# Kernel optimization log

Measured on AMD Instinct MI355X. Metric: run time of the kernel, lower is better.

## Reference

```python
import jax, jax.numpy as jnp
import numpy as np
import math

B, S, H = 2, 4096, 768
NH, HD = 12, 64  # num heads, head dim


def setup_inputs() -> dict:
    key = jax.random.key(0)
    ks = jax.random.split(key, 4)
    scale = 1.0 / math.sqrt(H)
    return {
        "hidden_states": jax.random.normal(ks[0], (B, S, H), jnp.float32),
        "attention_mask": jnp.zeros((B, 1, 1, S), jnp.float32),
        "Wq": jax.random.normal(ks[1], (H, H), jnp.float32) * scale,
        "bq": jnp.zeros((H,), jnp.float32),
        "Wk": jax.random.normal(ks[2], (H, H), jnp.float32) * scale,
        "bk": jnp.zeros((H,), jnp.float32),
        "Wv": jax.random.normal(ks[3], (H, H), jnp.float32) * scale,
        "bv": jnp.zeros((H,), jnp.float32),
    }


def reference(hidden_states, attention_mask, Wq, bq, Wk, bk, Wv, bv):
    # Linear projections (torch nn.Linear: x @ W.T + b)
    q = hidden_states @ Wq.T + bq  # [B,S,H]
    k = hidden_states @ Wk.T + bk
    v = hidden_states @ Wv.T + bv
    # split heads -> [B, NH, S, HD]
    def split(x):
        return x.reshape(B, S, NH, HD).transpose(0, 2, 1, 3)
    qh, kh, vh = split(q), split(k), split(v)
    scores = jnp.einsum('bhqd,bhkd->bhqk', qh, kh) / math.sqrt(HD)
    scores = scores + attention_mask  # additive mask, broadcast
    probs = jax.nn.softmax(scores, axis=-1)
    # dropout prob = 0.0 (inference) -> identity
    ctx = jnp.einsum('bhqk,bhkd->bhqd', probs, vh)
    ctx = ctx.transpose(0, 2, 1, 3).reshape(B, S, H)
    return ctx
```

## Files before the change

kernel.cpp:

```cpp
#include <hip/hip_runtime.h>
#include <hip/hip_bf16.h>

typedef float f32x4 __attribute__((ext_vector_type(4)));
typedef float f32x16 __attribute__((ext_vector_type(16)));
typedef short short8 __attribute__((ext_vector_type(8)));

#define LOG2E 1.44269504088896340736f

__device__ __forceinline__ ushort f2bf(float f){
  unsigned u = __builtin_bit_cast(unsigned, f);
  u = (u + 0x7fffu + ((u >> 16) & 1u)) >> 16;
  return (ushort)u;
}

__device__ __forceinline__ float exp2_hw(float x){
  float r; asm("v_exp_f32 %0, %1" : "=v"(r) : "v"(x)); return r;
}

__device__ __forceinline__ uint pack_bf16_rh(float lo, float hi){
  uint ul = __builtin_bit_cast(uint, lo) + 0x8000u;
  uint uh = __builtin_bit_cast(uint, hi) + 0x8000u;
  return __builtin_amdgcn_perm(uh, ul, 0x07060302u);
}

__device__ __forceinline__ float fmax3(float a, float b, float c){
  return fmaxf(fmaxf(a, b), c);
}

__global__ void cvt_kernel(const float* __restrict__ src, ushort* __restrict__ dst, int n4){
  int i = blockIdx.x * 256 + threadIdx.x;
  if (i < n4){
    float4 v = ((const float4*)src)[i];
    ushort4 o; o.x = f2bf(v.x); o.y = f2bf(v.y); o.z = f2bf(v.z); o.w = f2bf(v.w);
    ((ushort4*)dst)[i] = o;
  }
}

__global__ void scale_kernel(const float* __restrict__ src, float* __restrict__ dst,
                             float sc, int n){
  int i = blockIdx.x * 256 + threadIdx.x;
  if (i < n) dst[i] = src[i] * sc;
}

__global__ __launch_bounds__(256) void qkv_gemm(const ushort* __restrict__ Xb,
                                                const ushort* __restrict__ Wb,
                                                const float* __restrict__ bias,
                                                ushort* __restrict__ Out,
                                                float scale){
  __shared__ ushort Xs[128*64];
  __shared__ ushort Ws[128*64];
  const int m0 = blockIdx.x * 128, n0 = blockIdx.y * 128;
  const int tid = threadIdx.x, w = tid >> 6, lane = tid & 63;
  const int r = lane & 15, g = lane >> 4;
  const int wr = (w >> 1) * 64, wc = (w & 1) * 64;
  f32x4 acc[4][4] = {};
  for (int k0 = 0; k0 < 768; k0 += 64){
    #pragma unroll
    for (int p = 0; p < 4; p++){
      int c = tid + 256*p; int row = c >> 3, cir = c & 7;
      uint4 vx = *(const uint4*)(Xb + (size_t)(m0+row)*768 + k0 + cir*8);
      *(uint4*)((char*)Xs + row*128 + ((cir*16) ^ ((row&7)<<4))) = vx;
      uint4 vw = *(const uint4*)(Wb + (size_t)(n0+row)*768 + k0 + cir*8);
      *(uint4*)((char*)Ws + row*128 + ((cir*16) ^ ((row&7)<<4))) = vw;
    }
    __syncthreads();
    #pragma unroll
    for (int ks = 0; ks < 2; ks++){
      short8 af[4], bf[4];
      int bo = ks*64 + g*16;
      #pragma unroll
      for (int i = 0; i < 4; i++){
        int rowa = wr + i*16 + r;
        af[i] = *(const short8*)((char*)Xs + rowa*128 + (bo ^ ((rowa&7)<<4)));
        int rowb = wc + i*16 + r;
        bf[i] = *(const short8*)((char*)Ws + rowb*128 + (bo ^ ((rowb&7)<<4)));
      }
      #pragma unroll
      for (int i = 0; i < 4; i++)
        #pragma unroll
        for (int j = 0; j < 4; j++)
          acc[i][j] = __builtin_amdgcn_mfma_f32_16x16x32_bf16(af[i], bf[j], acc[i][j], 0,0,0);
    }
    __syncthreads();
  }
  #pragma unroll
  for (int i = 0; i < 4; i++){
    #pragma unroll
    for (int j = 0; j < 4; j++){
      int col = n0 + wc + j*16 + r;
      float bv = bias[col];
      int rowb = m0 + wr + i*16 + g*4;
      #pragma unroll
      for (int q = 0; q < 4; q++)
        Out[(size_t)(rowb+q)*768 + col] = f2bf((acc[i][j][q] + bv) * scale);
    }
  }
}

__global__ __launch_bounds__(256) void qkv_gemm_vt(const ushort* __restrict__ Xb,
                                                   const ushort* __restrict__ Wb,
                                                   const float* __restrict__ bias,
                                                   ushort* __restrict__ VtOut){
  __shared__ ushort Xs[128*64];
  __shared__ ushort Ws[128*64];
  const int m0 = blockIdx.x * 128, n0 = blockIdx.y * 128;
  const int tid = threadIdx.x, w = tid >> 6, lane = tid & 63;
  const int r = lane & 15, g = lane >> 4;
  const int wr = (w >> 1) * 64, wc = (w & 1) * 64;
  f32x4 acc[4][4] = {};
  for (int k0 = 0; k0 < 768; k0 += 64){
    #pragma unroll
    for (int p = 0; p < 4; p++){
      int c = tid + 256*p; int row = c >> 3, cir = c & 7;
      uint4 vx = *(const uint4*)(Xb + (size_t)(m0+row)*768 + k0 + cir*8);
      *(uint4*)((char*)Xs + row*128 + ((cir*16) ^ ((row&7)<<4))) = vx;
      uint4 vw = *(const uint4*)(Wb + (size_t)(n0+row)*768 + k0 + cir*8);
      *(uint4*)((char*)Ws + row*128 + ((cir*16) ^ ((row&7)<<4))) = vw;
    }
    __syncthreads();
    #pragma unroll
    for (int ks = 0; ks < 2; ks++){
      short8 af[4], bf[4];
      int bo = ks*64 + g*16;
      #pragma unroll
      for (int i = 0; i < 4; i++){
        int rowa = wr + i*16 + r;
        af[i] = *(const short8*)((char*)Xs + rowa*128 + (bo ^ ((rowa&7)<<4)));
        int rowb = wc + i*16 + r;
        bf[i] = *(const short8*)((char*)Ws + rowb*128 + (bo ^ ((rowb&7)<<4)));
      }
      #pragma unroll
      for (int i = 0; i < 4; i++)
        #pragma unroll
        for (int j = 0; j < 4; j++)
          acc[i][j] = __builtin_amdgcn_mfma_f32_16x16x32_bf16(af[i], bf[j], acc[i][j], 0,0,0);
    }
    __syncthreads();
  }
  #pragma unroll
  for (int i = 0; i < 4; i++){
    #pragma unroll
    for (int j = 0; j < 4; j++){
      int col = n0 + wc + j*16 + r;
      float bv = bias[col];
      int rowb = m0 + wr + i*16 + g*4;
      ushort4 o;
      o.x = f2bf(acc[i][j][0] + bv);
      o.y = f2bf(acc[i][j][1] + bv);
      o.z = f2bf(acc[i][j][2] + bv);
      o.w = f2bf(acc[i][j][3] + bv);
      size_t vrow = (size_t)((rowb >> 12) * 768 + col);
      *(ushort4*)(VtOut + vrow * 4096 + (rowb & 4095)) = o;
    }
  }
}

__global__ __launch_bounds__(256, 3) void flash_attn(const ushort* __restrict__ Qb,
                                                     const ushort* __restrict__ Kb,
                                                     const ushort* __restrict__ Vt,
                                                     const float* __restrict__ maskL,
                                                     float* __restrict__ out){
  __shared__ ushort Ks[64*64];
  __shared__ ushort Vts[64*64];
  const int tid = threadIdx.x, w = tid >> 6, lane = tid & 63;
  const int q = lane & 31, hi = lane >> 5;
  const int swq = (q & 7) << 4;
  const int h = blockIdx.y, b = blockIdx.z;
  const int q0 = blockIdx.x * 128 + w * 32;

  short8 bq[4];
  {
    const ushort* qp = Qb + (size_t)(b*4096 + q0 + q)*768 + h*64 + hi*8;
    #pragma unroll
    for (int kd = 0; kd < 4; kd++) bq[kd] = *(const short8*)(qp + 16*kd);
  }
  const ushort* Kbase = Kb + (size_t)(b*4096)*768 + h*64;
  const ushort* Vbase = Vt + (size_t)(b*768 + h*64)*4096;

  const int row0 = tid >> 3, cir = tid & 7;
  const int row1 = row0 + 32;

  uint4 kreg0, kreg1, vreg0, vreg1;
  kreg0 = *(const uint4*)(Kbase + (size_t)row0*768 + cir*8);
  kreg1 = *(const uint4*)(Kbase + (size_t)row1*768 + cir*8);
  vreg0 = *(const uint4*)(Vbase + (size_t)row0*4096 + cir*8);
  vreg1 = *(const uint4*)(Vbase + (size_t)row1*4096 + cir*8);

  f32x16 ctx[2] = {};
  float mrun = -1e30f, lrun = 0.f;

  for (int t = 0; t < 64; t++){
    const int kv0 = t * 64;
    *(uint4*)((char*)Ks  + row0*128 + ((cir*16) ^ ((row0&7)<<4))) = kreg0;
    *(uint4*)((char*)Ks  + row1*128 + ((cir*16) ^ ((row1&7)<<4))) = kreg1;
    *(uint4*)((char*)Vts + row0*128 + ((cir*16) ^ ((row0&7)<<4))) = vreg0;
    *(uint4*)((char*)Vts + row1*128 + ((cir*16) ^ ((row1&7)<<4))) = vreg1;
    __syncthreads();
    if (t < 63){
      const int kn = kv0 + 64;
      kreg0 = *(const uint4*)(Kbase + (size_t)(kn+row0)*768 + cir*8);
      kreg1 = *(const uint4*)(Kbase + (size_t)(kn+row1)*768 + cir*8);
      vreg0 = *(const uint4*)(Vbase + (size_t)row0*4096 + kn + cir*8);
      vreg1 = *(const uint4*)(Vbase + (size_t)row1*4096 + kn + cir*8);
    }
    f32x16 sc[2];
    #pragma unroll
    for (int s = 0; s < 2; s++){
      f32x16 z = {};
      #pragma unroll
      for (int kd = 0; kd < 4; kd++){
        int row = s*32 + q;
        short8 ak = *(const short8*)((char*)Ks + row*128 + ((32*kd + 16*hi) ^ swq));
        z = __builtin_amdgcn_mfma_f32_32x32x16_bf16(ak, bq[kd], z, 0,0,0);
      }
      sc[s] = z;
    }
    #pragma unroll
    for (int s = 0; s < 2; s++)
      #pragma unroll
      for (int eq = 0; eq < 4; eq++){
        float4 mv = *(const float4*)(maskL + b*4096 + kv0 + s*32 + eq*8 + hi*4);
        sc[s][4*eq+0] += mv.x; sc[s][4*eq+1] += mv.y;
        sc[s][4*eq+2] += mv.z; sc[s][4*eq+3] += mv.w;
      }
    float ma = fmax3(sc[0][0], sc[0][1], sc[0][2]);
    float mb = fmax3(sc[0][3], sc[0][4], sc[0][5]);
    ma = fmax3(ma, sc[0][6], sc[0][7]);
    mb = fmax3(mb, sc[0][8], sc[0][9]);
    ma = fmax3(ma, sc[0][10], sc[0][11]);
    mb = fmax3(mb, sc[0][12], sc[0][13]);
    ma = fmax3(ma, sc[0][14], sc[0][15]);
    #pragma unroll
    for (int e = 0; e < 15; e += 3) mb = fmax3(mb, sc[1][e], sc[1][e+1]);
    ma = fmax3(ma, sc[1][2], sc[1][5]);
    ma = fmax3(ma, sc[1][8], sc[1][11]);
    ma = fmax3(ma, sc[1][14], sc[1][15]);
    float mt = fmaxf(ma, mb);
    mt = fmaxf(mt, __shfl_xor(mt, 32, 64));
    if (!__all(mt <= mrun + 11.5415603f)){
      float mnew = fmaxf(mrun, mt);
      float alpha = exp2_hw(mrun - mnew);
      mrun = mnew;
      lrun *= alpha;
      #pragma unroll
      for (int s = 0; s < 2; s++)
        #pragma unroll
        for (int e = 0; e < 16; e++) ctx[s][e] *= alpha;
    }
    float rs = 0.f;
    #pragma unroll
    for (int s = 0; s < 2; s++)
      #pragma unroll
      for (int e = 0; e < 16; e++){
        float pv = exp2_hw(sc[s][e] - mrun); sc[s][e] = pv; rs += pv;
      }
    rs += __shfl_xor(rs, 32, 64);
    lrun += rs;
    short8 bp[4];
    #pragma unroll
    for (int s = 0; s < 2; s++){
      uint pw[8];
      #pragma unroll
      for (int u = 0; u < 8; u++)
        pw[u] = pack_bf16_rh(sc[s][2*u], sc[s][2*u+1]);
      #pragma unroll
      for (int u2 = 0; u2 < 2; u2++){
        uint x0 = pw[4*u2+0], x1 = pw[4*u2+1], x2 = pw[4*u2+2], x3 = pw[4*u2+3];
        asm("v_permlane32_swap_b32 %0, %1" : "+v"(x0), "+v"(x2));
        asm("v_permlane32_swap_b32 %0, %1" : "+v"(x1), "+v"(x3));
        union { uint u[4]; short8 v; } bb;
        bb.u[0] = x0; bb.u[1] = x1; bb.u[2] = x2; bb.u[3] = x3;
        bp[2*s + u2] = bb.v;
      }
    }
    #pragma unroll
    for (int sd = 0; sd < 2; sd++){
      int row = sd*32 + q;
      #pragma unroll
      for (int kk = 0; kk < 4; kk++){
        short8 av = *(const short8*)((char*)Vts + row*128 + ((32*kk + 16*hi) ^ swq));
        ctx[sd] = __builtin_amdgcn_mfma_f32_32x32x16_bf16(av, bp[kk], ctx[sd], 0,0,0);
      }
    }
    __syncthreads();
  }
  float inv = 1.0f / lrun;
  size_t orow = (size_t)(b*4096 + q0 + q) * 768 + h*64;
  #pragma unroll
  for (int sd = 0; sd < 2; sd++)
    #pragma unroll
    for (int eq = 0; eq < 4; eq++){
      float4 o;
      o.x = ctx[sd][4*eq+0] * inv; o.y = ctx[sd][4*eq+1] * inv;
      o.z = ctx[sd][4*eq+2] * inv; o.w = ctx[sd][4*eq+3] * inv;
      *(float4*)(out + orow + sd*32 + eq*8 + hi*4) = o;
    }
}

extern "C" void kernel_launch(void* const* d_in, const int* in_sizes, int n_in,
                              void* d_out, int out_size, void* d_ws, size_t ws_size,
                              hipStream_t stream){
  const float* hidden = (const float*)d_in[0];
  const float* mask   = (const float*)d_in[1];
  const float* Wq     = (const float*)d_in[2];
  const float* bq     = (const float*)d_in[3];
  const float* Wk     = (const float*)d_in[4];
  const float* bk     = (const float*)d_in[5];
  const float* Wv     = (const float*)d_in[6];
  const float* bv     = (const float*)d_in[7];
  char* ws = (char*)d_ws;
  ushort* Xb    = (ushort*)(ws);
  ushort* Wqb   = (ushort*)(ws + 12582912);
  ushort* Wkb   = (ushort*)(ws + 13762560);
  ushort* Wvb   = (ushort*)(ws + 14942208);
  ushort* Qb    = (ushort*)(ws + 16121856);
  ushort* Kb    = (ushort*)(ws + 28704768);
  ushort* Vtb   = (ushort*)(ws + 41287680);
  float*  maskL = (float*)(ws + 53870592);

  cvt_kernel<<<6144, 256, 0, stream>>>(hidden, Xb, 1572864);
  cvt_kernel<<<576, 256, 0, stream>>>(Wq, Wqb, 147456);
  cvt_kernel<<<576, 256, 0, stream>>>(Wk, Wkb, 147456);
  cvt_kernel<<<576, 256, 0, stream>>>(Wv, Wvb, 147456);
  scale_kernel<<<32, 256, 0, stream>>>(mask, maskL, LOG2E, 8192);

  dim3 gg(64, 6);
  qkv_gemm<<<gg, 256, 0, stream>>>(Xb, Wqb, bq, Qb, 0.125f * LOG2E);
  qkv_gemm<<<gg, 256, 0, stream>>>(Xb, Wkb, bk, Kb, 1.0f);
  qkv_gemm_vt<<<gg, 256, 0, stream>>>(Xb, Wvb, bv, Vtb);

  dim3 ga(32, 12, 2);
  flash_attn<<<ga, 256, 0, stream>>>(Qb, Kb, Vtb, maskL, (float*)d_out);
}
```

Before: 240.6 us.

## Double-buffer K/V in LDS, use packed FP32 math, and direct global-to-LDS loads in GEMM

The attention kernel now keeps two LDS buffers for K/Vt and prefetches two tiles ahead, so it needs one barrier per iteration instead of two. It also uses v_pk_add/v_pk_mul for the mask add, max subtraction and rescale, hardware v_cvt_pk_bf16_f32 for packing, and s_setprio around the MFMA blocks. The QKV GEMMs replace register-staged loads with global_load_lds direct-to-LDS transfers, applying the swizzle on the source side. LDS use doubles to 32KB per block, which may reduce occupancy. The bf16 rounding also changes from the round-half-up bit trick to the hardware conversion.

```diff
diff --git a/kernel.cpp b/kernel.cpp
--- a/kernel.cpp
+++ b/kernel.cpp
@@ -17,15 +17,23 @@
   float r; asm("v_exp_f32 %0, %1" : "=v"(r) : "v"(x)); return r;
 }
 
-__device__ __forceinline__ uint pack_bf16_rh(float lo, float hi){
-  uint ul = __builtin_bit_cast(uint, lo) + 0x8000u;
-  uint uh = __builtin_bit_cast(uint, hi) + 0x8000u;
-  return __builtin_amdgcn_perm(uh, ul, 0x07060302u);
-}
-
+__device__ __forceinline__ double pk_add(double a, double b){
+  double d; asm("v_pk_add_f32 %0, %1, %2" : "=v"(d) : "v"(a), "v"(b)); return d;
+}
+__device__ __forceinline__ double pk_mul(double a, double b){
+  double d; asm("v_pk_mul_f32 %0, %1, %2" : "=v"(d) : "v"(a), "v"(b)); return d;
+}
+__device__ __forceinline__ uint cvtpk_bf16(float lo, float hi){
+  uint r; asm("v_cvt_pk_bf16_f32 %0, %1, %2" : "=v"(r) : "v"(lo), "v"(hi)); return r;
+}
+__device__ __forceinline__ double f2d(float x, float y){
+  union { float f[2]; double d; } u; u.f[0] = x; u.f[1] = y; return u.d;
+}
 __device__ __forceinline__ float fmax3(float a, float b, float c){
   return fmaxf(fmaxf(a, b), c);
 }
+
+union F16u { f32x16 v; double d[8]; float f[16]; };
 
 __global__ void cvt_kernel(const float* __restrict__ src, ushort* __restrict__ dst, int n4){
   int i = blockIdx.x * 256 + threadIdx.x;
@@ -53,15 +61,20 @@
   const int tid = threadIdx.x, w = tid >> 6, lane = tid & 63;
   const int r = lane & 15, g = lane >> 4;
   const int wr = (w >> 1) * 64, wc = (w & 1) * 64;
+  const int lrow = lane >> 3;
+  const int gk = (lane & 7) ^ lrow;
   f32x4 acc[4][4] = {};
   for (int k0 = 0; k0 < 768; k0 += 64){
     #pragma unroll
     for (int p = 0; p < 4; p++){
-      int c = tid + 256*p; int row = c >> 3, cir = c & 7;
-      uint4 vx = *(const uint4*)(Xb + (size_t)(m0+row)*768 + k0 + cir*8);
-      *(uint4*)((char*)Xs + row*128 + ((cir*16) ^ ((row&7)<<4))) = vx;
-      uint4 vw = *(const uint4*)(Wb + (size_t)(n0+row)*768 + k0 + cir*8);
-      *(uint4*)((char*)Ws + row*128 + ((cir*16) ^ ((row&7)<<4))) = vw;
+      int rowb = p*32 + w*8;
+      int row = rowb + lrow;
+      __builtin_amdgcn_global_load_lds(
+        (const uint4*)(Xb + (size_t)(m0+row)*768 + k0 + gk*8),
+        (uint4*)((char*)Xs + rowb*128), 16, 0, 0);
+      __builtin_amdgcn_global_load_lds(
+        (const uint4*)(Wb + (size_t)(n0+row)*768 + k0 + gk*8),
+        (uint4*)((char*)Ws + rowb*128), 16, 0, 0);
     }
     __syncthreads();
     #pragma unroll
@@ -72,8 +85,8 @@
       for (int i = 0; i < 4; i++){
         int rowa = wr + i*16 + r;
         af[i] = *(const short8*)((char*)Xs + rowa*128 + (bo ^ ((rowa&7)<<4)));
-        int rowb = wc + i*16 + r;
-        bf[i] = *(const short8*)((char*)Ws + rowb*128 + (bo ^ ((rowb&7)<<4)));
+        int rowb2 = wc + i*16 + r;
+        bf[i] = *(const short8*)((char*)Ws + rowb2*128 + (bo ^ ((rowb2&7)<<4)));
       }
       #pragma unroll
       for (int i = 0; i < 4; i++)
@@ -107,15 +120,20 @@
   const int tid = threadIdx.x, w = tid >> 6, lane = tid & 63;
   const int r = lane & 15, g = lane >> 4;
   const int wr = (w >> 1) * 64, wc = (w & 1) * 64;
+  const int lrow = lane >> 3;
+  const int gk = (lane & 7) ^ lrow;
   f32x4 acc[4][4] = {};
   for (int k0 = 0; k0 < 768; k0 += 64){
     #pragma unroll
     for (int p = 0; p < 4; p++){
-      int c = tid + 256*p; int row = c >> 3, cir = c & 7;
-      uint4 vx = *(const uint4*)(Xb + (size_t)(m0+row)*768 + k0 + cir*8);
-      *(uint4*)((char*)Xs + row*128 + ((cir*16) ^ ((row&7)<<4))) = vx;
-      uint4 vw = *(const uint4*)(Wb + (size_t)(n0+row)*768 + k0 + cir*8);
-      *(uint4*)((char*)Ws + row*128 + ((cir*16) ^ ((row&7)<<4))) = vw;
+      int rowb = p*32 + w*8;
+      int row = rowb + lrow;
+      __builtin_amdgcn_global_load_lds(
+        (const uint4*)(Xb + (size_t)(m0+row)*768 + k0 + gk*8),
+        (uint4*)((char*)Xs + rowb*128), 16, 0, 0);
+      __builtin_amdgcn_global_load_lds(
+        (const uint4*)(Wb + (size_t)(n0+row)*768 + k0 + gk*8),
+        (uint4*)((char*)Ws + rowb*128), 16, 0, 0);
     }
     __syncthreads();
     #pragma unroll
@@ -126,8 +144,8 @@
       for (int i = 0; i < 4; i++){
         int rowa = wr + i*16 + r;
         af[i] = *(const short8*)((char*)Xs + rowa*128 + (bo ^ ((rowa&7)<<4)));
-        int rowb = wc + i*16 + r;
-        bf[i] = *(const short8*)((char*)Ws + rowb*128 + (bo ^ ((rowb&7)<<4)));
+        int rowb2 = wc + i*16 + r;
+        bf[i] = *(const short8*)((char*)Ws + rowb2*128 + (bo ^ ((rowb2&7)<<4)));
       }
       #pragma unroll
       for (int i = 0; i < 4; i++)
@@ -160,13 +178,13 @@
                                                      const ushort* __restrict__ Vt,
                                                      const float* __restrict__ maskL,
                                                      float* __restrict__ out){
-  __shared__ ushort Ks[64*64];
-  __shared__ ushort Vts[64*64];
+  __shared__ ushort SM[16384];
   const int tid = threadIdx.x, w = tid >> 6, lane = tid & 63;
   const int q = lane & 31, hi = lane >> 5;
   const int swq = (q & 7) << 4;
   const int h = blockIdx.y, b = blockIdx.z;
   const int q0 = blockIdx.x * 128 + w * 32;
+  char* sm = (char*)SM;
 
   short8 bq[4];
   {
@@ -179,90 +197,131 @@
 
   const int row0 = tid >> 3, cir = tid & 7;
   const int row1 = row0 + 32;
-
-  uint4 kreg0, kreg1, vreg0, vreg1;
-  kreg0 = *(const uint4*)(Kbase + (size_t)row0*768 + cir*8);
-  kreg1 = *(const uint4*)(Kbase + (size_t)row1*768 + cir*8);
-  vreg0 = *(const uint4*)(Vbase + (size_t)row0*4096 + cir*8);
-  vreg1 = *(const uint4*)(Vbase + (size_t)row1*4096 + cir*8);
-
-  f32x16 ctx[2] = {};
+  const int wb0 = row0*128 + ((cir*16) ^ ((row0&7)<<4));
+  const int wb1 = row1*128 + ((cir*16) ^ ((row1&7)<<4));
+  const ushort* kp0 = Kbase + (size_t)row0*768 + cir*8;
+  const ushort* kp1 = Kbase + (size_t)row1*768 + cir*8;
+  const ushort* vp0 = Vbase + (size_t)row0*4096 + cir*8;
+  const ushort* vp1 = Vbase + (size_t)row1*4096 + cir*8;
+
+  int off8[8];
+  #pragma unroll
+  for (int s = 0; s < 2; s++)
+    #pragma unroll
+    for (int kd = 0; kd < 4; kd++)
+      off8[s*4+kd] = (s*32 + q)*128 + ((32*kd + 16*hi) ^ swq);
+
+  uint4 k0r = *(const uint4*)kp0, k1r = *(const uint4*)kp1;
+  uint4 v0r = *(const uint4*)vp0, v1r = *(const uint4*)vp1;
+  *(uint4*)(sm + wb0) = k0r;           *(uint4*)(sm + wb1) = k1r;
+  *(uint4*)(sm + 16384 + wb0) = v0r;   *(uint4*)(sm + 16384 + wb1) = v1r;
+  k0r = *(const uint4*)(kp0 + (size_t)64*768);
+  k1r = *(const uint4*)(kp1 + (size_t)64*768);
+  v0r = *(const uint4*)(vp0 + 64);
+  v1r = *(const uint4*)(vp1 + 64);
+  __syncthreads();
+
+  F16u c0, c1;
+  { f32x16 zz = {}; c0.v = zz; c1.v = zz; }
   float mrun = -1e30f, lrun = 0.f;
 
   for (int t = 0; t < 64; t++){
-    const int kv0 = t * 64;
-    *(uint4*)((char*)Ks  + row0*128 + ((cir*16) ^ ((row0&7)<<4))) = kreg0;
-    *(uint4*)((char*)Ks  + row1*128 + ((cir*16) ^ ((row1&7)<<4))) = kreg1;
-    *(uint4*)((char*)Vts + row0*128 + ((cir*16) ^ ((row0&7)<<4))) = vreg0;
-    *(uint4*)((char*)Vts + row1*128 + ((cir*16) ^ ((row1&7)<<4))) = vreg1;
-    __syncthreads();
+    const int tb = (t & 1) << 13;
+    const char* kb = sm + tb;
+    const char* vb = kb + 16384;
+    __builtin_amdgcn_s_setprio(1);
+    f32x16 z0 = {}, z1 = {};
+    #pragma unroll
+    for (int kd = 0; kd < 4; kd++){
+      short8 ak = *(const short8*)(kb + off8[kd]);
+      z0 = __builtin_amdgcn_mfma_f32_32x32x16_bf16(ak, bq[kd], z0, 0,0,0);
+    }
+    #pragma unroll
+    for (int kd = 0; kd < 4; kd++){
+      short8 ak = *(const short8*)(kb + off8[4+kd]);
+      z1 = __builtin_amdgcn_mfma_f32_32x32x16_bf16(ak, bq[kd], z1, 0,0,0);
+    }
+    __builtin_amdgcn_s_setprio(0);
+    F16u s0, s1; s0.v = z0; s1.v = z1;
     if (t < 63){
-      const int kn = kv0 + 64;
-      kreg0 = *(const uint4*)(Kbase + (size_t)(kn+row0)*768 + cir*8);
-      kreg1 = *(const uint4*)(Kbase + (size_t)(kn+row1)*768 + cir*8);
-      vreg0 = *(const uint4*)(Vbase + (size_t)row0*4096 + kn + cir*8);
-      vreg1 = *(const uint4*)(Vbase + (size_t)row1*4096 + kn + cir*8);
-    }
-    f32x16 sc[2];
-    #pragma unroll
-    for (int s = 0; s < 2; s++){
-      f32x16 z = {};
-      #pragma unroll
-      for (int kd = 0; kd < 4; kd++){
-        int row = s*32 + q;
-        short8 ak = *(const short8*)((char*)Ks + row*128 + ((32*kd + 16*hi) ^ swq));
-        z = __builtin_amdgcn_mfma_f32_32x32x16_bf16(ak, bq[kd], z, 0,0,0);
-      }
-      sc[s] = z;
-    }
-    #pragma unroll
-    for (int s = 0; s < 2; s++)
-      #pragma unroll
-      for (int eq = 0; eq < 4; eq++){
-        float4 mv = *(const float4*)(maskL + b*4096 + kv0 + s*32 + eq*8 + hi*4);
-        sc[s][4*eq+0] += mv.x; sc[s][4*eq+1] += mv.y;
-        sc[s][4*eq+2] += mv.z; sc[s][4*eq+3] += mv.w;
-      }
-    float ma = fmax3(sc[0][0], sc[0][1], sc[0][2]);
-    float mb = fmax3(sc[0][3], sc[0][4], sc[0][5]);
-    ma = fmax3(ma, sc[0][6], sc[0][7]);
-    mb = fmax3(mb, sc[0][8], sc[0][9]);
-    ma = fmax3(ma, sc[0][10], sc[0][11]);
-    mb = fmax3(mb, sc[0][12], sc[0][13]);
-    ma = fmax3(ma, sc[0][14], sc[0][15]);
-    #pragma unroll
-    for (int e = 0; e < 15; e += 3) mb = fmax3(mb, sc[1][e], sc[1][e+1]);
-    ma = fmax3(ma, sc[1][2], sc[1][5]);
-    ma = fmax3(ma, sc[1][8], sc[1][11]);
-    ma = fmax3(ma, sc[1][14], sc[1][15]);
-    float mt = fmaxf(ma, mb);
+      char* wbuf = sm + (tb ^ 8192);
+      *(uint4*)(wbuf + wb0) = k0r;           *(uint4*)(wbuf + wb1) = k1r;
+      *(uint4*)(wbuf + 16384 + wb0) = v0r;   *(uint4*)(wbuf + 16384 + wb1) = v1r;
+    }
+    if (t < 62){
+      const size_t kn = (size_t)(t+2) * 64;
+      k0r = *(const uint4*)(kp0 + kn*768);
+      k1r = *(const uint4*)(kp1 + kn*768);
+      v0r = *(const uint4*)(vp0 + kn);
+      v1r = *(const uint4*)(vp1 + kn);
+    }
+    const float* mrow = maskL + b*4096 + t*64 + hi*4;
+    #pragma unroll
+    for (int eq = 0; eq < 4; eq++){
+      float4 m0v = *(const float4*)(mrow + eq*8);
+      s0.d[2*eq]   = pk_add(s0.d[2*eq],   f2d(m0v.x, m0v.y));
+      s0.d[2*eq+1] = pk_add(s0.d[2*eq+1], f2d(m0v.z, m0v.w));
+      float4 m1v = *(const float4*)(mrow + 32 + eq*8);
+      s1.d[2*eq]   = pk_add(s1.d[2*eq],   f2d(m1v.x, m1v.y));
+      s1.d[2*eq+1] = pk_add(s1.d[2*eq+1], f2d(m1v.z, m1v.w));
+    }
+    float ma = fmax3(s0.f[0], s0.f[1], s0.f[2]);
+    float mb = fmax3(s0.f[3], s0.f[4], s0.f[5]);
+    ma = fmax3(ma, s0.f[6], s0.f[7]);
+    mb = fmax3(mb, s0.f[8], s0.f[9]);
+    ma = fmax3(ma, s0.f[10], s0.f[11]);
+    mb = fmax3(mb, s0.f[12], s0.f[13]);
+    ma = fmax3(ma, s0.f[14], s0.f[15]);
+    mb = fmax3(mb, s1.f[0], s1.f[1]);
+    ma = fmax3(ma, s1.f[2], s1.f[3]);
+    mb = fmax3(mb, s1.f[4], s1.f[5]);
+    ma = fmax3(ma, s1.f[6], s1.f[7]);
+    mb = fmax3(mb, s1.f[8], s1.f[9]);
+    ma = fmax3(ma, s1.f[10], s1.f[11]);
+    mb = fmax3(mb, s1.f[12], s1.f[13]);
+    float mt = fmax3(ma, s1.f[14], fmaxf(mb, s1.f[15]));
     mt = fmaxf(mt, __shfl_xor(mt, 32, 64));
     if (!__all(mt <= mrun + 11.5415603f)){
       float mnew = fmaxf(mrun, mt);
       float alpha = exp2_hw(mrun - mnew);
       mrun = mnew;
       lrun *= alpha;
-      #pragma unroll
-      for (int s = 0; s < 2; s++)
-        #pragma unroll
-        for (int e = 0; e < 16; e++) ctx[s][e] *= alpha;
-    }
-    float rs = 0.f;
-    #pragma unroll
-    for (int s = 0; s < 2; s++)
-      #pragma unroll
-      for (int e = 0; e < 16; e++){
-        float pv = exp2_hw(sc[s][e] - mrun); sc[s][e] = pv; rs += pv;
+      double al2 = f2d(alpha, alpha);
+      #pragma unroll
+      for (int i = 0; i < 8; i++){
+        c0.d[i] = pk_mul(c0.d[i], al2);
+        c1.d[i] = pk_mul(c1.d[i], al2);
       }
-    rs += __shfl_xor(rs, 32, 64);
-    lrun += rs;
+    }
+    double msub = f2d(-mrun, -mrun);
+    #pragma unroll
+    for (int i = 0; i < 8; i++){
+      s0.d[i] = pk_add(s0.d[i], msub);
+      s1.d[i] = pk_add(s1.d[i], msub);
+    }
+    #pragma unroll
+    for (int e = 0; e < 16; e++){
+      s0.f[e] = exp2_hw(s0.f[e]);
+      s1.f[e] = exp2_hw(s1.f[e]);
+    }
+    double t00 = pk_add(s0.d[0], s0.d[1]), t01 = pk_add(s0.d[2], s0.d[3]);
+    double t02 = pk_add(s0.d[4], s0.d[5]), t03 = pk_add(s0.d[6], s0.d[7]);
+    double t10 = pk_add(s1.d[0], s1.d[1]), t11 = pk_add(s1.d[2], s1.d[3]);
+    double t12 = pk_add(s1.d[4], s1.d[5]), t13 = pk_add(s1.d[6], s1.d[7]);
+    double u0 = pk_add(t00, t01), u1 = pk_add(t02, t03);
+    double u2 = pk_add(t10, t11), u3 = pk_add(t12, t13);
+    double wsum = pk_add(pk_add(u0, u1), pk_add(u2, u3));
+    {
+      union { double d; float f[2]; } uw; uw.d = wsum;
+      float rs = uw.f[0] + uw.f[1];
+      rs += __shfl_xor(rs, 32, 64);
+      lrun += rs;
+    }
     short8 bp[4];
-    #pragma unroll
-    for (int s = 0; s < 2; s++){
+    {
       uint pw[8];
       #pragma unroll
-      for (int u = 0; u < 8; u++)
-        pw[u] = pack_bf16_rh(sc[s][2*u], sc[s][2*u+1]);
+      for (int u = 0; u < 8; u++) pw[u] = cvtpk_bf16(s0.f[2*u], s0.f[2*u+1]);
       #pragma unroll
       for (int u2 = 0; u2 < 2; u2++){
         uint x0 = pw[4*u2+0], x1 = pw[4*u2+1], x2 = pw[4*u2+2], x3 = pw[4*u2+3];
@@ -270,31 +329,50 @@
         asm("v_permlane32_swap_b32 %0, %1" : "+v"(x1), "+v"(x3));
         union { uint u[4]; short8 v; } bb;
         bb.u[0] = x0; bb.u[1] = x1; bb.u[2] = x2; bb.u[3] = x3;
-        bp[2*s + u2] = bb.v;
+        bp[u2] = bb.v;
       }
-    }
-    #pragma unroll
-    for (int sd = 0; sd < 2; sd++){
-      int row = sd*32 + q;
-      #pragma unroll
-      for (int kk = 0; kk < 4; kk++){
-        short8 av = *(const short8*)((char*)Vts + row*128 + ((32*kk + 16*hi) ^ swq));
-        ctx[sd] = __builtin_amdgcn_mfma_f32_32x32x16_bf16(av, bp[kk], ctx[sd], 0,0,0);
+      #pragma unroll
+      for (int u = 0; u < 8; u++) pw[u] = cvtpk_bf16(s1.f[2*u], s1.f[2*u+1]);
+      #pragma unroll
+      for (int u2 = 0; u2 < 2; u2++){
+        uint x0 = pw[4*u2+0], x1 = pw[4*u2+1], x2 = pw[4*u2+2], x3 = pw[4*u2+3];
+        asm("v_permlane32_swap_b32 %0, %1" : "+v"(x0), "+v"(x2));
+        asm("v_permlane32_swap_b32 %0, %1" : "+v"(x1), "+v"(x3));
+        union { uint u[4]; short8 v; } bb;
+        bb.u[0] = x0; bb.u[1] = x1; bb.u[2] = x2; bb.u[3] = x3;
+        bp[2+u2] = bb.v;
       }
     }
+    __builtin_amdgcn_s_setprio(1);
+    #pragma unroll
+    for (int kk = 0; kk < 4; kk++){
+      short8 av = *(const short8*)(vb + off8[kk]);
+      c0.v = __builtin_amdgcn_mfma_f32_32x32x16_bf16(av, bp[kk], c0.v, 0,0,0);
+    }
+    #pragma unroll
+    for (int kk = 0; kk < 4; kk++){
+      short8 av = *(const short8*)(vb + off8[4+kk]);
+      c1.v = __builtin_amdgcn_mfma_f32_32x32x16_bf16(av, bp[kk], c1.v, 0,0,0);
+    }
+    __builtin_amdgcn_s_setprio(0);
     __syncthreads();
   }
   float inv = 1.0f / lrun;
   size_t orow = (size_t)(b*4096 + q0 + q) * 768 + h*64;
   #pragma unroll
-  for (int sd = 0; sd < 2; sd++)
-    #pragma unroll
-    for (int eq = 0; eq < 4; eq++){
-      float4 o;
-      o.x = ctx[sd][4*eq+0] * inv; o.y = ctx[sd][4*eq+1] * inv;
-      o.z = ctx[sd][4*eq+2] * inv; o.w = ctx[sd][4*eq+3] * inv;
-      *(float4*)(out + orow + sd*32 + eq*8 + hi*4) = o;
-    }
+  for (int eq = 0; eq < 4; eq++){
+    float4 o;
+    o.x = c0.f[4*eq+0] * inv; o.y = c0.f[4*eq+1] * inv;
+    o.z = c0.f[4*eq+2] * inv; o.w = c0.f[4*eq+3] * inv;
+    *(float4*)(out + orow + eq*8 + hi*4) = o;
+  }
+  #pragma unroll
+  for (int eq = 0; eq < 4; eq++){
+    float4 o;
+    o.x = c1.f[4*eq+0] * inv; o.y = c1.f[4*eq+1] * inv;
+    o.z = c1.f[4*eq+2] * inv; o.w = c1.f[4*eq+3] * inv;
+    *(float4*)(out + orow + 32 + eq*8 + hi*4) = o;
+  }
 }
 
 extern "C" void kernel_launch(void* const* d_in, const int* in_sizes, int n_in,
```

Measured after the change: 231.1 us. 3.9% less time.
